# Optimization experiments

Hardware: AMD Instinct MI355X
Metric: run time of the kernel (lower is better)

## Reference

```python
import jax, jax.numpy as jnp
import numpy as np

B, S, H = 4, 2048, 512
I = 1024  # intermediate_dim
E = 8     # num_experts
K = 2     # top_k


def setup_inputs() -> dict:
    key = jax.random.key(0)
    k1, k2, k3, k4 = jax.random.split(key, 4)
    x = jax.random.normal(k1, (B, S, H), dtype=jnp.float32)
    expert_indices = jax.random.randint(k2, (B, S, K), 0, E, dtype=jnp.int32)
    # parameters: init.normal_(std=0.02)
    w13 = 0.02 * jax.random.normal(k3, (E, H, 2 * I), dtype=jnp.float32)
    w2 = 0.02 * jax.random.normal(k4, (E, I, H), dtype=jnp.float32)
    return {"x": x, "expert_indices": expert_indices, "w13": w13, "w2": w2}


def reference(x, expert_indices, w13, w2):
    # x: (B,S,H); expert_indices: (B,S,K); w13: (E,H,2I); w2: (E,I,H)
    # Same math as torch's per-token weight gather + matmul, expressed as
    # dense all-expert GEMM followed by per-token expert selection.
    h13_all = jnp.einsum('bsh,ehd->bsed', x, w13)          # (B,S,E,2I)
    h13 = jnp.take_along_axis(h13_all, expert_indices[..., None], axis=2)  # (B,S,K,2I)
    gate, up = jnp.split(h13, 2, axis=-1)                   # each (B,S,K,I)
    h_inter = jax.nn.silu(gate) * up                        # (B,S,K,I)
    out_all = jnp.einsum('bski,eih->bskeh', h_inter, w2)    # (B,S,K,E,H)
    out = jnp.take_along_axis(out_all, expert_indices[..., None, None], axis=3)
    return out.squeeze(3)                                   # (B,S,K,H)
```

## Files before the change

kernel.cpp:

```cpp
#include <hip/hip_runtime.h>


#define H_DIM 512
#define I_DIM 1024
#define E_NUM 8
#define P_PAIRS 16384
#define CAP P_PAIRS
#define MAX_TILES 136

#define PREP_TW13 2048
#define PREP_TW2 1024
#define PREP_CVT 2048
#define PREP_ROUTE 64
#define PREP_BLOCKS (PREP_TW13 + PREP_TW2 + PREP_CVT + PREP_ROUTE)

typedef _Float16 half8 __attribute__((ext_vector_type(8)));
typedef float f32x4 __attribute__((ext_vector_type(4)));
typedef unsigned int u32;
typedef const __attribute__((address_space(1))) u32* gas_t;
typedef __attribute__((address_space(3))) u32* las_t;

__device__ __forceinline__ void glds16(const void* g, void* l) {
  __builtin_amdgcn_global_load_lds((gas_t)g, (las_t)l, 16, 0, 0);
}

__device__ __forceinline__ bool tile_decode(const int* counts, int ty, int& e,
                                            int& m0, int& ne, int& rb) {
  int base = 0;
  rb = 0;
  for (e = 0; e < E_NUM; ++e) {
    ne = counts[e];
    const int nt = (ne + 127) >> 7;
    if (ty < base + nt) { m0 = (ty - base) << 7; return true; }
    base += nt;
    rb += ne;
  }
  return false;
}

__global__ __launch_bounds__(256) void prep_k(
    const float* __restrict__ x, const int* __restrict__ idx,
    const float* __restrict__ w13, const float* __restrict__ w2,
    int* __restrict__ counts, int* __restrict__ lists,
    _Float16* __restrict__ xh, _Float16* __restrict__ w13t,
    _Float16* __restrict__ w2t) {
  __shared__ __align__(16) _Float16 tile[64][72];
  const int b = blockIdx.x;
  const int tid = threadIdx.x;

  if (b < PREP_TW13 + PREP_TW2) {
    const float* src;
    _Float16* dst;
    int R, C, c0, r0;
    if (b < PREP_TW13) {
      R = H_DIM; C = 2 * I_DIM;
      const int e = b >> 8;
      c0 = (b & 31) * 64;
      r0 = ((b >> 5) & 7) * 64;
      src = w13 + (size_t)e * R * C;
      dst = w13t + (size_t)e * C * R;
    } else {
      const int l = b - PREP_TW13;
      R = I_DIM; C = H_DIM;
      const int e = l >> 7;
      c0 = (l & 7) * 64;
      r0 = ((l >> 3) & 15) * 64;
      src = w2 + (size_t)e * R * C;
      dst = w2t + (size_t)e * C * R;
    }
    {
      const int r = tid >> 4;
      const int c4 = (tid & 15) * 4;
      for (int pass = 0; pass < 4; ++pass) {
        f32x4 v = *(const f32x4*)(src + (size_t)(r0 + pass * 16 + r) * C + c0 + c4);
        for (int j = 0; j < 4; ++j) tile[c4 + j][pass * 16 + r] = (_Float16)v[j];
      }
    }
    __syncthreads();
    {
      const int c = tid >> 3;
      const int r8 = (tid & 7) * 8;
      for (int pass = 0; pass < 2; ++pass) {
        half8 h = *(const half8*)&tile[pass * 32 + c][r8];
        *(half8*)(dst + (size_t)(c0 + pass * 32 + c) * R + r0 + r8) = h;
      }
    }
  } else if (b < PREP_TW13 + PREP_TW2 + PREP_CVT) {
    const int l = b - (PREP_TW13 + PREP_TW2);
    const size_t i = ((size_t)l * 256 + tid) * 8;
    f32x4 v0 = *(const f32x4*)(x + i);
    f32x4 v1 = *(const f32x4*)(x + i + 4);
    half8 h;
    for (int j = 0; j < 4; ++j) { h[j] = (_Float16)v0[j]; h[j + 4] = (_Float16)v1[j]; }
    *(half8*)(xh + i) = h;
  } else {
    int* lcnt = (int*)&tile[0][0];
    int* lbase = lcnt + E_NUM;
    const int l = b - (PREP_TW13 + PREP_TW2 + PREP_CVT);
    if (tid < E_NUM) lcnt[tid] = 0;
    __syncthreads();
    const int p = l * 256 + tid;
    const int e = idx[p];
    const int r = atomicAdd(&lcnt[e], 1);
    __syncthreads();
    if (tid < E_NUM) lbase[tid] = atomicAdd(&counts[tid], lcnt[tid]);
    __syncthreads();
    lists[e * CAP + lbase[e] + r] = p;
  }
}

__global__ __launch_bounds__(256) void gemm1_k(
    const _Float16* __restrict__ xh, const _Float16* __restrict__ w13t,
    const int* __restrict__ counts, const int* __restrict__ lists,
    _Float16* __restrict__ h_ws) {
  int e, m0, ne, rb;
  if (!tile_decode(counts, blockIdx.y, e, m0, ne, rb)) return;
  const int n0 = blockIdx.x * 64;

  __shared__ int rows[128];
  __shared__ __align__(16) _Float16 As[128 * 32];
  __shared__ __align__(16) _Float16 Bgs[64 * 32];
  __shared__ __align__(16) _Float16 Bus[64 * 32];

  const int tid = threadIdx.x;
  if (tid < 128) {
    const int m = m0 + tid;
    rows[tid] = (m < ne) ? lists[e * CAP + m] : -1;
  }
  __syncthreads();

  const int sr = tid >> 2;
  const int s4 = tid & 3;
  const int segoff = ((s4 ^ ((sr >> 1) & 3)) * 8);
  const int pa0 = rows[sr];
  const int pa1 = rows[64 + sr];
  const int t0 = (pa0 >= 0) ? (pa0 >> 1) : 0;
  const int t1 = (pa1 >= 0) ? (pa1 >> 1) : 0;
  const _Float16* ga0 = xh + (size_t)t0 * H_DIM + segoff;
  const _Float16* ga1 = xh + (size_t)t1 * H_DIM + segoff;
  const _Float16* gbg = w13t + ((size_t)e * 2 * I_DIM + n0 + sr) * H_DIM + segoff;
  const _Float16* gbu = gbg + (size_t)I_DIM * H_DIM;
  _Float16* la0 = As + sr * 32 + s4 * 8;
  _Float16* la1 = As + (64 + sr) * 32 + s4 * 8;
  _Float16* lbg = Bgs + sr * 32 + s4 * 8;
  _Float16* lbu = Bus + sr * 32 + s4 * 8;

  const int lane = tid & 63;
  const int wid = tid >> 6;
  const int wm = wid & 1;
  const int wn = wid >> 1;
  const int fm = lane & 15;
  const int q = lane >> 4;
  int aoff[4], boff[2];
  for (int mi = 0; mi < 4; ++mi) {
    const int rA = wm * 64 + mi * 16 + fm;
    aoff[mi] = rA * 32 + ((q ^ ((rA >> 1) & 3)) * 8);
  }
  for (int ni = 0; ni < 2; ++ni) {
    const int cB = wn * 32 + ni * 16 + fm;
    boff[ni] = cB * 32 + ((q ^ ((cB >> 1) & 3)) * 8);
  }

  f32x4 accg[4][2] = {};
  f32x4 accu[4][2] = {};

  for (int k0 = 0; k0 < H_DIM; k0 += 32) {
    glds16(ga0 + k0, la0);
    glds16(ga1 + k0, la1);
    glds16(gbg + k0, lbg);
    glds16(gbu + k0, lbu);
    __syncthreads();

    half8 af[4], bg[2], bu[2];
    for (int mi = 0; mi < 4; ++mi) af[mi] = *(const half8*)&As[aoff[mi]];
    for (int ni = 0; ni < 2; ++ni) {
      bg[ni] = *(const half8*)&Bgs[boff[ni]];
      bu[ni] = *(const half8*)&Bus[boff[ni]];
    }
    for (int mi = 0; mi < 4; ++mi)
      for (int ni = 0; ni < 2; ++ni) {
        accg[mi][ni] = __builtin_amdgcn_mfma_f32_16x16x32_f16(af[mi], bg[ni], accg[mi][ni], 0, 0, 0);
        accu[mi][ni] = __builtin_amdgcn_mfma_f32_16x16x32_f16(af[mi], bu[ni], accu[mi][ni], 0, 0, 0);
      }
    __syncthreads();
  }

  for (int mi = 0; mi < 4; ++mi)
    for (int r = 0; r < 4; ++r) {
      const int mrow = wm * 64 + mi * 16 + q * 4 + r;
      if (m0 + mrow >= ne) continue;
      _Float16* hrow = h_ws + (size_t)(rb + m0 + mrow) * I_DIM + n0;
      for (int ni = 0; ni < 2; ++ni) {
        const int c = wn * 32 + ni * 16 + fm;
        const float g = accg[mi][ni][r];
        const float u = accu[mi][ni][r];
        hrow[c] = (_Float16)(g / (1.0f + __expf(-g)) * u);
      }
    }
}

__global__ __launch_bounds__(256) void gemm2_k(
    const _Float16* __restrict__ h_ws, const _Float16* __restrict__ w2t,
    const int* __restrict__ counts, const int* __restrict__ lists,
    float* __restrict__ out) {
  int e, m0, ne, rb;
  if (!tile_decode(counts, blockIdx.x, e, m0, ne, rb)) return;
  const int n0 = blockIdx.y * 64;

  __shared__ int rows[128];
  __shared__ __align__(16) _Float16 As[128 * 32];
  __shared__ __align__(16) _Float16 Bs[64 * 32];

  const int tid = threadIdx.x;
  if (tid < 128) {
    const int m = m0 + tid;
    rows[tid] = (m < ne) ? lists[e * CAP + m] : -1;
  }

  const int sr = tid >> 2;
  const int s4 = tid & 3;
  const int segoff = ((s4 ^ ((sr >> 1) & 3)) * 8);
  int grow0 = rb + m0 + sr;
  int grow1 = rb + m0 + 64 + sr;
  if (grow0 > P_PAIRS - 1) grow0 = P_PAIRS - 1;
  if (grow1 > P_PAIRS - 1) grow1 = P_PAIRS - 1;
  const _Float16* ga0 = h_ws + (size_t)grow0 * I_DIM + segoff;
  const _Float16* ga1 = h_ws + (size_t)grow1 * I_DIM + segoff;
  const _Float16* gb = w2t + ((size_t)e * H_DIM + n0 + sr) * I_DIM + segoff;
  _Float16* la0 = As + sr * 32 + s4 * 8;
  _Float16* la1 = As + (64 + sr) * 32 + s4 * 8;
  _Float16* lb = Bs + sr * 32 + s4 * 8;

  const int lane = tid & 63;
  const int wid = tid >> 6;
  const int wm = wid & 1;
  const int wn = wid >> 1;
  const int fm = lane & 15;
  const int q = lane >> 4;
  int aoff[4], boff[2];
  for (int mi = 0; mi < 4; ++mi) {
    const int rA = wm * 64 + mi * 16 + fm;
    aoff[mi] = rA * 32 + ((q ^ ((rA >> 1) & 3)) * 8);
  }
  for (int ni = 0; ni < 2; ++ni) {
    const int cB = wn * 32 + ni * 16 + fm;
    boff[ni] = cB * 32 + ((q ^ ((cB >> 1) & 3)) * 8);
  }

  f32x4 acc[4][2] = {};

  for (int k0 = 0; k0 < I_DIM; k0 += 32) {
    glds16(ga0 + k0, la0);
    glds16(ga1 + k0, la1);
    glds16(gb + k0, lb);
    __syncthreads();

    half8 af[4], bf[2];
    for (int mi = 0; mi < 4; ++mi) af[mi] = *(const half8*)&As[aoff[mi]];
    for (int ni = 0; ni < 2; ++ni) bf[ni] = *(const half8*)&Bs[boff[ni]];
    for (int mi = 0; mi < 4; ++mi)
      for (int ni = 0; ni < 2; ++ni)
        acc[mi][ni] = __builtin_amdgcn_mfma_f32_16x16x32_f16(af[mi], bf[ni], acc[mi][ni], 0, 0, 0);
    __syncthreads();
  }

  for (int mi = 0; mi < 4; ++mi)
    for (int r = 0; r < 4; ++r) {
      const int mrow = wm * 64 + mi * 16 + q * 4 + r;
      const int p = rows[mrow];
      if (p < 0) continue;
      float* orow = out + (size_t)p * H_DIM + n0;
      for (int ni = 0; ni < 2; ++ni)
        orow[wn * 32 + ni * 16 + fm] = acc[mi][ni][r];
    }
}

extern "C" void kernel_launch(void* const* d_in, const int* in_sizes, int n_in,
                              void* d_out, int out_size, void* d_ws, size_t ws_size,
                              hipStream_t stream) {
  const float* x = (const float*)d_in[0];
  const int* idx = (const int*)d_in[1];
  const float* w13 = (const float*)d_in[2];
  const float* w2 = (const float*)d_in[3];

  char* ws = (char*)d_ws;
  int* counts = (int*)ws;
  int* lists = (int*)(ws + 2048);
  const size_t OFF_XH = 2048 + (size_t)E_NUM * CAP * 4;
  const size_t OFF_W13T = OFF_XH + (size_t)P_PAIRS / 2 * H_DIM * 2;
  const size_t OFF_W2T = OFF_W13T + (size_t)E_NUM * 2 * I_DIM * H_DIM * 2;
  const size_t OFF_H = OFF_W2T + (size_t)E_NUM * H_DIM * I_DIM * 2;
  _Float16* xh = (_Float16*)(ws + OFF_XH);
  _Float16* w13t = (_Float16*)(ws + OFF_W13T);
  _Float16* w2t = (_Float16*)(ws + OFF_W2T);
  _Float16* h_ws = (_Float16*)(ws + OFF_H);

  hipMemsetAsync(d_ws, 0, 128, stream);
  prep_k<<<dim3(PREP_BLOCKS), 256, 0, stream>>>(x, idx, w13, w2, counts, lists,
                                                xh, w13t, w2t);
  gemm1_k<<<dim3(I_DIM / 64, MAX_TILES), 256, 0, stream>>>(
      xh, w13t, counts, lists, h_ws);
  gemm2_k<<<dim3(MAX_TILES, H_DIM / 64), 256, 0, stream>>>(
      h_ws, w2t, counts, lists, (float*)d_out);
}
```

Baseline: 205.4 us.

## Double-buffer gemm2 LDS staging and vectorize output stores via swapped MFMA operands

Result: faster. 200.6 us (-2.4%).

```diff
diff --git a/kernel.cpp b/kernel.cpp
--- a/kernel.cpp
+++ b/kernel.cpp
@@ -208,8 +208,8 @@
   const int n0 = blockIdx.y * 64;
 
   __shared__ int rows[128];
-  __shared__ __align__(16) _Float16 As[128 * 32];
-  __shared__ __align__(16) _Float16 Bs[64 * 32];
+  __shared__ __align__(16) _Float16 As[2][128 * 32];
+  __shared__ __align__(16) _Float16 Bs[2][64 * 32];
 
   const int tid = threadIdx.x;
   if (tid < 128) {
@@ -227,9 +227,9 @@
   const _Float16* ga0 = h_ws + (size_t)grow0 * I_DIM + segoff;
   const _Float16* ga1 = h_ws + (size_t)grow1 * I_DIM + segoff;
   const _Float16* gb = w2t + ((size_t)e * H_DIM + n0 + sr) * I_DIM + segoff;
-  _Float16* la0 = As + sr * 32 + s4 * 8;
-  _Float16* la1 = As + (64 + sr) * 32 + s4 * 8;
-  _Float16* lb = Bs + sr * 32 + s4 * 8;
+  const int lA0 = sr * 32 + s4 * 8;
+  const int lA1 = (64 + sr) * 32 + s4 * 8;
+  const int lB = sr * 32 + s4 * 8;
 
   const int lane = tid & 63;
   const int wid = tid >> 6;
@@ -249,30 +249,44 @@
 
   f32x4 acc[4][2] = {};
 
-  for (int k0 = 0; k0 < I_DIM; k0 += 32) {
-    glds16(ga0 + k0, la0);
-    glds16(ga1 + k0, la1);
-    glds16(gb + k0, lb);
-    __syncthreads();
-
-    half8 af[4], bf[2];
-    for (int mi = 0; mi < 4; ++mi) af[mi] = *(const half8*)&As[aoff[mi]];
-    for (int ni = 0; ni < 2; ++ni) bf[ni] = *(const half8*)&Bs[boff[ni]];
-    for (int mi = 0; mi < 4; ++mi)
-      for (int ni = 0; ni < 2; ++ni)
-        acc[mi][ni] = __builtin_amdgcn_mfma_f32_16x16x32_f16(af[mi], bf[ni], acc[mi][ni], 0, 0, 0);
-    __syncthreads();
-  }
-
-  for (int mi = 0; mi < 4; ++mi)
-    for (int r = 0; r < 4; ++r) {
-      const int mrow = wm * 64 + mi * 16 + q * 4 + r;
-      const int p = rows[mrow];
-      if (p < 0) continue;
-      float* orow = out + (size_t)p * H_DIM + n0;
-      for (int ni = 0; ni < 2; ++ni)
-        orow[wn * 32 + ni * 16 + fm] = acc[mi][ni][r];
-    }
+#define G2_STAGE(buf, k0)                      \
+  do {                                         \
+    glds16(ga0 + (k0), &As[buf][lA0]);         \
+    glds16(ga1 + (k0), &As[buf][lA1]);         \
+    glds16(gb + (k0), &Bs[buf][lB]);           \
+  } while (0)
+
+#define G2_COMPUTE(buf)                                                          \
+  do {                                                                           \
+    half8 af[4], bf[2];                                                          \
+    for (int mi = 0; mi < 4; ++mi) af[mi] = *(const half8*)&As[buf][aoff[mi]];   \
+    for (int ni = 0; ni < 2; ++ni) bf[ni] = *(const half8*)&Bs[buf][boff[ni]];   \
+    for (int mi = 0; mi < 4; ++mi)                                               \
+      for (int ni = 0; ni < 2; ++ni)                                             \
+        acc[mi][ni] = __builtin_amdgcn_mfma_f32_16x16x32_f16(                    \
+            bf[ni], af[mi], acc[mi][ni], 0, 0, 0);                               \
+  } while (0)
+
+  G2_STAGE(0, 0);
+  __syncthreads();
+  for (int k0 = 0; k0 < I_DIM; k0 += 64) {
+    G2_STAGE(1, k0 + 32);
+    G2_COMPUTE(0);
+    __syncthreads();
+    if (k0 + 64 < I_DIM) G2_STAGE(0, k0 + 64);
+    G2_COMPUTE(1);
+    __syncthreads();
+  }
+#undef G2_STAGE
+#undef G2_COMPUTE
+
+  for (int mi = 0; mi < 4; ++mi) {
+    const int p = rows[wm * 64 + mi * 16 + fm];
+    if (p < 0) continue;
+    float* orow = out + (size_t)p * H_DIM + n0;
+    for (int ni = 0; ni < 2; ++ni)
+      *(f32x4*)&orow[wn * 32 + ni * 16 + q * 4] = acc[mi][ni];
+  }
 }
 
 extern "C" void kernel_launch(void* const* d_in, const int* in_sizes, int n_in,
```
